# Kernel tuning notes

Hardware: AMD Instinct MI355X
Metric: run time of the kernel (lower is better)

Reference implementation:

```python
import jax, jax.numpy as jnp
import numpy as np

N_NODES = 50000
N_EDGES = 400000
IN_CH = 109
OUT_CH = 32


def setup_inputs() -> dict:
    key = jax.random.key(0)
    ks = jax.random.split(key, 12)
    dims = [(IN_CH, 10 * OUT_CH), (10 * OUT_CH, 2 * OUT_CH), (2 * OUT_CH, OUT_CH), (2 * OUT_CH, OUT_CH)]
    inp = {
        'x': jax.random.normal(ks[0], (N_NODES, IN_CH), dtype=jnp.float32),
        'edge_index': jax.random.randint(ks[1], (2, N_EDGES), 0, N_NODES, dtype=jnp.int64) if jax.config.jax_enable_x64 else jax.random.randint(ks[1], (2, N_EDGES), 0, N_NODES, dtype=jnp.int32),
    }
    names = ['W1', 'b1', 'W2', 'b2', 'Wmu', 'bmu', 'Wls', 'bls']
    for i, (fi, fo) in enumerate(dims):
        scale = 1.0 / np.sqrt(fi)
        inp[names[2 * i]] = jax.random.uniform(ks[2 + 2 * i], (fi, fo), minval=-scale, maxval=scale, dtype=jnp.float32)
        inp[names[2 * i + 1]] = jnp.zeros((fo,), dtype=jnp.float32)
    return inp


def _gcn_conv(x, src, dst, norm, W, b, n):
    # PyG GCNConv: h = x @ W, then symmetric-normalized aggregation, then + b
    h = x @ W                                   # [N, F_out]
    msg = h[src] * norm[:, None]                # [E+N, F_out]
    out = jax.ops.segment_sum(msg, dst, num_segments=n)
    return out + b


def _norm_and_loops(edge_index, n):
    # add self loops, compute D^{-1/2}(A+I)D^{-1/2} edge weights
    loops = jnp.arange(n, dtype=edge_index.dtype)
    src = jnp.concatenate([edge_index[0], loops])
    dst = jnp.concatenate([edge_index[1], loops])
    deg = jax.ops.segment_sum(jnp.ones_like(src, dtype=jnp.float32), dst, num_segments=n)
    dinv = jnp.where(deg > 0, jax.lax.rsqrt(jnp.maximum(deg, 1.0)), 0.0)
    norm = dinv[src] * dinv[dst]
    return src, dst, norm


def reference(x, edge_index, W1, b1, W2, b2, Wmu, bmu, Wls, bls):
    n = x.shape[0]
    src, dst, norm = _norm_and_loops(edge_index, n)
    h = jax.nn.relu(_gcn_conv(x, src, dst, norm, W1, b1, n))
    h = jax.nn.relu(_gcn_conv(h, src, dst, norm, W2, b2, n))
    mu = _gcn_conv(h, src, dst, norm, Wmu, bmu, n)
    logstd = _gcn_conv(h, src, dst, norm, Wls, bls, n)
    return (mu, logstd)
```

## Files before the change

### kernel.cpp

```cpp
#include <hip/hip_runtime.h>

#define NN 50000
#define NE 400000

typedef __attribute__((ext_vector_type(8))) short short8v;
typedef __attribute__((ext_vector_type(4))) float f32x4;

__device__ __forceinline__ unsigned short f2bf_rtn(float x) {
    unsigned u = __float_as_uint(x);
    unsigned r = u + 0x7FFFu + ((u >> 16) & 1u);
    return (unsigned short)(r >> 16);
}
__device__ __forceinline__ float bf2f(unsigned short h) {
    return __uint_as_float(((unsigned)h) << 16);
}

__global__ void prep_kernel(const float* __restrict__ x,
                            const float* __restrict__ W1, const float* __restrict__ W2,
                            const float* __restrict__ Wmu, const float* __restrict__ Wls,
                            unsigned* __restrict__ xp, int* __restrict__ zero_base,
                            unsigned short* __restrict__ w1t_hi,
                            unsigned short* __restrict__ w2t_hi, unsigned short* __restrict__ w2t_lo,
                            unsigned short* __restrict__ wct_hi, unsigned short* __restrict__ wct_lo) {
    int b = blockIdx.x, tid = threadIdx.x;
    if (b < 12500) {
        int idx = b * 256 + tid;
        int i = idx >> 6, c2 = (idx & 63) * 2;
        long xb = (long)i * 109;
        float v0 = (c2 < 109) ? x[xb + c2] : 0.0f;
        float v1 = (c2 + 1 < 109) ? x[xb + c2 + 1] : 0.0f;
        xp[idx] = (unsigned)f2bf_rtn(v0) | ((unsigned)f2bf_rtn(v1) << 16);
    } else if (b < 12891) {
        int i = (b - 12500) * 256 + tid;
        if (i < 100096) zero_base[i] = 0;
    } else if (b < 13051) {
        int idx = (b - 12891) * 256 + tid;
        int n = idx >> 7, k = idx & 127;
        float v = (k < 109) ? W1[(long)k * 320 + n] : 0.0f;
        w1t_hi[idx] = f2bf_rtn(v);
    } else if (b < 13131) {
        int idx = (b - 13051) * 256 + tid;
        int n = idx / 320, k = idx - n * 320;
        float v = W2[(long)k * 64 + n];
        unsigned short hb = f2bf_rtn(v);
        w2t_hi[idx] = hb;
        w2t_lo[idx] = f2bf_rtn(v - bf2f(hb));
    } else {
        int idx = (b - 13131) * 256 + tid;
        int n = idx >> 6, k = idx & 63;
        float v = (n < 32) ? Wmu[k * 32 + n] : Wls[k * 32 + (n - 32)];
        unsigned short hb = f2bf_rtn(v);
        wct_hi[idx] = hb;
        wct_lo[idx] = f2bf_rtn(v - bf2f(hb));
    }
}

__global__ void hist_kernel(const int* __restrict__ dst, int* __restrict__ counts) {
    for (int e = blockIdx.x * blockDim.x + threadIdx.x; e < NE; e += gridDim.x * blockDim.x)
        atomicAdd(&counts[dst[e]], 1);
}

__global__ void dinv_scan1_kernel(const int* __restrict__ counts, float* __restrict__ dinv,
                                  int* __restrict__ rowstart, int* __restrict__ bsum) {
    __shared__ int tmp[256];
    int tid = threadIdx.x;
    int i = blockIdx.x * 256 + tid;
    int v = (i < NN) ? counts[i] : 0;
    if (i < NN) dinv[i] = rsqrtf((float)(v + 1));
    tmp[tid] = v;
    __syncthreads();
    for (int off = 1; off < 256; off <<= 1) {
        int t = 0;
        if (tid >= off) t = tmp[tid - off];
        __syncthreads();
        if (tid >= off) tmp[tid] += t;
        __syncthreads();
    }
    if (i < NN) rowstart[i] = tmp[tid] - v;
    if (tid == 255) bsum[blockIdx.x] = tmp[255];
}

__global__ void scan23_kernel(int* __restrict__ rowstart, const int* __restrict__ bsum) {
    __shared__ int red[4];
    int tid = threadIdx.x;
    int v = (tid < 196 && tid < (int)blockIdx.x) ? bsum[tid] : 0;
    for (int off = 32; off > 0; off >>= 1) v += __shfl_down(v, off, 64);
    if ((tid & 63) == 0) red[tid >> 6] = v;
    __syncthreads();
    int pref = red[0] + red[1] + red[2] + red[3];
    int i = blockIdx.x * 256 + tid;
    if (i < NN) rowstart[i] += pref;
    if (i == 0) rowstart[NN] = NE;
}

__global__ void scatter_kernel(const int* __restrict__ src, const int* __restrict__ dst,
                               const int* __restrict__ rowstart, int* __restrict__ cursor,
                               int* __restrict__ esrc) {
    for (int e = blockIdx.x * blockDim.x + threadIdx.x; e < NE; e += gridDim.x * blockDim.x) {
        int d = dst[e];
        int pos = rowstart[d] + atomicAdd(&cursor[d], 1);
        esrc[pos] = src[e];
    }
}

__global__ __launch_bounds__(256) void agg109_packed_kernel(const int* __restrict__ rowstart,
                                                            const int* __restrict__ esrc,
                                                            const float* __restrict__ dinv,
                                                            const unsigned* __restrict__ xp,
                                                            unsigned* __restrict__ xa_hi32) {
    int wave = blockIdx.x * (blockDim.x >> 6) + (threadIdx.x >> 6);
    if (wave >= NN) return;
    int lane = threadIdx.x & 63;
    float wd = dinv[wave];
    unsigned pself = xp[(long)wave * 64 + lane];
    float acc0 = __uint_as_float(pself << 16) * wd;
    float acc1 = __uint_as_float(pself & 0xFFFF0000u) * wd;
    int j0 = rowstart[wave], j1 = rowstart[wave + 1];
    int j = j0;
    for (; j + 8 <= j1; j += 8) {
        int s[8];
        float w[8];
        unsigned pp[8];
        #pragma unroll
        for (int u = 0; u < 8; ++u) s[u] = esrc[j + u];
        #pragma unroll
        for (int u = 0; u < 8; ++u) w[u] = dinv[s[u]];
        #pragma unroll
        for (int u = 0; u < 8; ++u) pp[u] = xp[(long)s[u] * 64 + lane];
        #pragma unroll
        for (int u = 0; u < 8; ++u) {
            acc0 = fmaf(__uint_as_float(pp[u] << 16), w[u], acc0);
            acc1 = fmaf(__uint_as_float(pp[u] & 0xFFFF0000u), w[u], acc1);
        }
    }
    for (; j + 4 <= j1; j += 4) {
        int s0 = esrc[j], s1 = esrc[j + 1], s2 = esrc[j + 2], s3 = esrc[j + 3];
        float w0 = dinv[s0], w1 = dinv[s1], w2 = dinv[s2], w3 = dinv[s3];
        unsigned p0 = xp[(long)s0 * 64 + lane], p1 = xp[(long)s1 * 64 + lane];
        unsigned p2 = xp[(long)s2 * 64 + lane], p3 = xp[(long)s3 * 64 + lane];
        acc0 = fmaf(__uint_as_float(p0 << 16), w0, acc0);
        acc1 = fmaf(__uint_as_float(p0 & 0xFFFF0000u), w0, acc1);
        acc0 = fmaf(__uint_as_float(p1 << 16), w1, acc0);
        acc1 = fmaf(__uint_as_float(p1 & 0xFFFF0000u), w1, acc1);
        acc0 = fmaf(__uint_as_float(p2 << 16), w2, acc0);
        acc1 = fmaf(__uint_as_float(p2 & 0xFFFF0000u), w2, acc1);
        acc0 = fmaf(__uint_as_float(p3 << 16), w3, acc0);
        acc1 = fmaf(__uint_as_float(p3 & 0xFFFF0000u), w3, acc1);
    }
    for (; j < j1; ++j) {
        int s = esrc[j];
        float w = dinv[s];
        unsigned pv = xp[(long)s * 64 + lane];
        acc0 = fmaf(__uint_as_float(pv << 16), w, acc0);
        acc1 = fmaf(__uint_as_float(pv & 0xFFFF0000u), w, acc1);
    }
    acc0 *= wd;
    acc1 *= wd;
    xa_hi32[(long)wave * 64 + lane] =
        (unsigned)f2bf_rtn(acc0) | ((unsigned)f2bf_rtn(acc1) << 16);
}

__global__ __launch_bounds__(256) void agg64_relu_bf16_kernel(const int* __restrict__ rowstart,
                                                              const int* __restrict__ esrc,
                                                              const float* __restrict__ dinv,
                                                              const unsigned short* __restrict__ g,
                                                              const float* __restrict__ b,
                                                              unsigned short* __restrict__ hhi) {
    int wave = blockIdx.x * (blockDim.x >> 6) + (threadIdx.x >> 6);
    if (wave >= NN) return;
    int lane = threadIdx.x & 63;
    long base = (long)wave * 64;
    float acc = bf2f(g[base + lane]);
    int j0 = rowstart[wave], j1 = rowstart[wave + 1];
    int j = j0;
    for (; j + 4 <= j1; j += 4) {
        int s0 = esrc[j], s1 = esrc[j + 1], s2 = esrc[j + 2], s3 = esrc[j + 3];
        float p0 = bf2f(g[(long)s0 * 64 + lane]), p1 = bf2f(g[(long)s1 * 64 + lane]);
        float p2 = bf2f(g[(long)s2 * 64 + lane]), p3 = bf2f(g[(long)s3 * 64 + lane]);
        acc += p0 + p1 + p2 + p3;
    }
    for (; j < j1; ++j) acc += bf2f(g[(long)esrc[j] * 64 + lane]);
    float v = acc * dinv[wave] + b[lane];
    v = v > 0.0f ? v : 0.0f;
    hhi[base + lane] = f2bf_rtn(v);
}

__global__ __launch_bounds__(256) void agg64b_kernel(const int* __restrict__ rowstart,
                                                     const int* __restrict__ esrc,
                                                     const float* __restrict__ dinv,
                                                     const unsigned short* __restrict__ h,
                                                     unsigned short* __restrict__ a_hi) {
    int wave = blockIdx.x * (blockDim.x >> 6) + (threadIdx.x >> 6);
    if (wave >= NN) return;
    int lane = threadIdx.x & 63;
    long base = (long)wave * 64;
    float wd = dinv[wave];
    float acc = bf2f(h[base + lane]) * wd;
    int j0 = rowstart[wave], j1 = rowstart[wave + 1];
    int j = j0;
    for (; j + 4 <= j1; j += 4) {
        int s0 = esrc[j], s1 = esrc[j + 1], s2 = esrc[j + 2], s3 = esrc[j + 3];
        float w0 = dinv[s0], w1 = dinv[s1], w2 = dinv[s2], w3 = dinv[s3];
        float p0 = bf2f(h[(long)s0 * 64 + lane]), p1 = bf2f(h[(long)s1 * 64 + lane]);
        float p2 = bf2f(h[(long)s2 * 64 + lane]), p3 = bf2f(h[(long)s3 * 64 + lane]);
        acc = fmaf(p0, w0, acc); acc = fmaf(p1, w1, acc);
        acc = fmaf(p2, w2, acc); acc = fmaf(p3, w3, acc);
    }
    for (; j < j1; ++j) {
        int s = esrc[j];
        acc = fmaf(bf2f(h[(long)s * 64 + lane]), dinv[s], acc);
    }
    a_hi[base + lane] = f2bf_rtn(acc * wd);
}

#define LDT 72

template <int MODE>
__global__ __launch_bounds__(256) void mfma_gemm_kernel(
    const unsigned short* __restrict__ Ahi,
    const unsigned short* __restrict__ Bhi, const unsigned short* __restrict__ Blo,
    const float* __restrict__ bias, const float* __restrict__ bias2,
    const float* __restrict__ dinv,
    unsigned short* __restrict__ Chi,
    float* __restrict__ Cf, int M, int N, int K, int grid_n) {
    constexpr bool BLO = (MODE != 0);
    __shared__ unsigned short As[64 * LDT];
    __shared__ unsigned short Bs[(BLO ? 2 : 1) * 64 * LDT];
    int tid = threadIdx.x;
    int wid = tid >> 6, lane = tid & 63;
    int l15 = lane & 15, l4 = lane >> 4;

    int T = gridDim.x;
    int xcd = blockIdx.x & 7, jj = blockIdx.x >> 3;
    int q = T >> 3, r = T & 7;
    int start = (xcd < r) ? xcd * (q + 1) : r * (q + 1) + (xcd - r) * q;
    int lin = start + jj;
    int bm = lin / grid_n, bn = lin - bm * grid_n;
    int bm0 = bm * 64, bn0 = bn * 64;

    f32x4 acc[4] = {};

    for (int kc = 0; kc < K; kc += 64) {
        #pragma unroll
        for (int r2 = 0; r2 < 2; ++r2) {
            int idx = tid + 256 * r2;
            int row = idx >> 3, slot = idx & 7;
            int grow = bm0 + row;
            if (grow >= M) grow = M - 1;
            long go = (long)grow * K + kc + slot * 8;
            *(uint4*)&As[row * LDT + slot * 8] = *(const uint4*)&Ahi[go];
            long gob = (long)(bn0 + row) * K + kc + slot * 8;
            *(uint4*)&Bs[row * LDT + slot * 8] = *(const uint4*)&Bhi[gob];
            if (BLO) *(uint4*)&Bs[64 * LDT + row * LDT + slot * 8] = *(const uint4*)&Blo[gob];
        }
        __syncthreads();
        #pragma unroll
        for (int ks = 0; ks < 2; ++ks) {
            int koff = ks * 32 + l4 * 8;
            int ra = (wid * 16 + l15) * LDT + koff;
            short8v ah = *(const short8v*)&As[ra];
            #pragma unroll
            for (int n = 0; n < 4; ++n) {
                int rb = (n * 16 + l15) * LDT + koff;
                short8v bh = *(const short8v*)&Bs[rb];
                acc[n] = __builtin_amdgcn_mfma_f32_16x16x32_bf16(ah, bh, acc[n], 0, 0, 0);
                if (BLO) {
                    short8v bl = *(const short8v*)&Bs[64 * LDT + rb];
                    acc[n] = __builtin_amdgcn_mfma_f32_16x16x32_bf16(ah, bl, acc[n], 0, 0, 0);
                }
            }
        }
        __syncthreads();
    }
    int rbase = bm0 + wid * 16 + l4 * 4;
    #pragma unroll
    for (int q2 = 0; q2 < 4; ++q2) {
        int grow = rbase + q2;
        if (grow >= M) continue;
        float rs = (MODE == 1) ? dinv[grow] : 0.0f;
        #pragma unroll
        for (int n = 0; n < 4; ++n) {
            int gcol = bn0 + n * 16 + l15;
            float v = acc[n][q2];
            if (MODE == 0) {
                v += bias[gcol];
                v = v > 0.0f ? v : 0.0f;
                Chi[(long)grow * N + gcol] = f2bf_rtn(v);
            } else if (MODE == 1) {
                Chi[(long)grow * N + gcol] = f2bf_rtn(v * rs);
            } else {
                if (gcol < 32)
                    Cf[(long)grow * 32 + gcol] = v + bias[gcol];
                else
                    Cf[(long)NN * 32 + (long)grow * 32 + (gcol - 32)] = v + bias2[gcol - 32];
            }
        }
    }
}

extern "C" void kernel_launch(void* const* d_in, const int* in_sizes, int n_in,
                              void* d_out, int out_size, void* d_ws, size_t ws_size,
                              hipStream_t stream) {
    const float* x   = (const float*)d_in[0];
    const int*   ei  = (const int*)d_in[1];
    const int*   src = ei;
    const int*   dst = ei + NE;
    const float* W1  = (const float*)d_in[2];
    const float* b1  = (const float*)d_in[3];
    const float* W2  = (const float*)d_in[4];
    const float* b2  = (const float*)d_in[5];
    const float* Wmu = (const float*)d_in[6];
    const float* bmu = (const float*)d_in[7];
    const float* Wls = (const float*)d_in[8];
    const float* bls = (const float*)d_in[9];
    float* out = (float*)d_out;

    char* p = (char*)d_ws;
    float* dinv   = (float*)p; p += 50048 * 4;
    int* counts   = (int*)p;   p += 50048 * 4;
    int* cursor   = (int*)p;   p += 50048 * 4;
    int* rowstart = (int*)p;   p += 50056 * 4;
    int* bsum     = (int*)p;   p += 256 * 4;
    int* esrc     = (int*)p;   p += 400000 * 4;
    unsigned* xp          = (unsigned*)p;       p += 50000L * 64 * 4;
    unsigned short* xa_hi = (unsigned short*)p; p += 50000L * 128 * 2;
    unsigned short* a2_hi = (unsigned short*)p; p += 50000L * 64 * 2;
    unsigned short* g2b   = (unsigned short*)p; p += 50000L * 64 * 2;
    unsigned short* h1_hi = (unsigned short*)p; p += 50000L * 320 * 2;
    unsigned short* w1t_hi = (unsigned short*)p; p += 320 * 128 * 2;
    unsigned short* w2t_hi = (unsigned short*)p; p += 64 * 320 * 2;
    unsigned short* w2t_lo = (unsigned short*)p; p += 64 * 320 * 2;
    unsigned short* wct_hi = (unsigned short*)p; p += 64 * 64 * 2;
    unsigned short* wct_lo = (unsigned short*)p; p += 64 * 64 * 2;
    unsigned short* h2_hi = xa_hi;

    const int TB = 256;
    const int NB_NODES = (NN + TB - 1) / TB;
    const int NB_AGG = (NN * 64 + TB - 1) / TB;

    prep_kernel<<<13147, TB, 0, stream>>>(x, W1, W2, Wmu, Wls, xp, counts,
                                          w1t_hi, w2t_hi, w2t_lo, wct_hi, wct_lo);
    hist_kernel<<<1024, TB, 0, stream>>>(dst, counts);
    dinv_scan1_kernel<<<NB_NODES, TB, 0, stream>>>(counts, dinv, rowstart, bsum);
    scan23_kernel<<<NB_NODES, TB, 0, stream>>>(rowstart, bsum);
    scatter_kernel<<<1024, TB, 0, stream>>>(src, dst, rowstart, cursor, esrc);

    agg109_packed_kernel<<<NB_AGG, TB, 0, stream>>>(rowstart, esrc, dinv, xp,
                                                    (unsigned*)xa_hi);
    mfma_gemm_kernel<0><<<782 * 5, 256, 0, stream>>>(xa_hi, w1t_hi, nullptr, b1,
                                                     nullptr, nullptr, h1_hi, nullptr,
                                                     NN, 320, 128, 5);

    mfma_gemm_kernel<1><<<782, 256, 0, stream>>>(h1_hi, w2t_hi, w2t_lo, nullptr,
                                                 nullptr, dinv, g2b, nullptr,
                                                 NN, 64, 320, 1);
    agg64_relu_bf16_kernel<<<NB_AGG, TB, 0, stream>>>(rowstart, esrc, dinv, g2b, b2, h2_hi);

    agg64b_kernel<<<NB_AGG, TB, 0, stream>>>(rowstart, esrc, dinv, h2_hi, a2_hi);
    mfma_gemm_kernel<3><<<782, 256, 0, stream>>>(a2_hi, wct_hi, wct_lo, bmu,
                                                 bls, nullptr, nullptr, out,
                                                 NN, 64, 64, 1);
}
```

Before: 177.9 us.

## Drop bf16 lo-split weights in GEMMs and unroll aggregation loops by eight

Removes the hi/lo bf16 split of the W2 and fused mu/logstd weights, so those GEMMs run one MFMA per fragment instead of two and load half the B data into shared memory. Separately, the two 64-wide aggregation kernels get an 8-way unrolled gather loop to keep more independent loads in flight. The precision drop adds rounding error to the weights, which could loosen accuracy against the fp32 reference.

```diff
diff --git a/kernel.cpp b/kernel.cpp
--- a/kernel.cpp
+++ b/kernel.cpp
@@ -20,8 +20,8 @@
                             const float* __restrict__ Wmu, const float* __restrict__ Wls,
                             unsigned* __restrict__ xp, int* __restrict__ zero_base,
                             unsigned short* __restrict__ w1t_hi,
-                            unsigned short* __restrict__ w2t_hi, unsigned short* __restrict__ w2t_lo,
-                            unsigned short* __restrict__ wct_hi, unsigned short* __restrict__ wct_lo) {
+                            unsigned short* __restrict__ w2t_hi,
+                            unsigned short* __restrict__ wct_hi) {
     int b = blockIdx.x, tid = threadIdx.x;
     if (b < 12500) {
         int idx = b * 256 + tid;
@@ -41,17 +41,12 @@
     } else if (b < 13131) {
         int idx = (b - 13051) * 256 + tid;
         int n = idx / 320, k = idx - n * 320;
-        float v = W2[(long)k * 64 + n];
-        unsigned short hb = f2bf_rtn(v);
-        w2t_hi[idx] = hb;
-        w2t_lo[idx] = f2bf_rtn(v - bf2f(hb));
+        w2t_hi[idx] = f2bf_rtn(W2[(long)k * 64 + n]);
     } else {
         int idx = (b - 13131) * 256 + tid;
         int n = idx >> 6, k = idx & 63;
         float v = (n < 32) ? Wmu[k * 32 + n] : Wls[k * 32 + (n - 32)];
-        unsigned short hb = f2bf_rtn(v);
-        wct_hi[idx] = hb;
-        wct_lo[idx] = f2bf_rtn(v - bf2f(hb));
+        wct_hi[idx] = f2bf_rtn(v);
     }
 }
 
@@ -173,6 +168,16 @@
     float acc = bf2f(g[base + lane]);
     int j0 = rowstart[wave], j1 = rowstart[wave + 1];
     int j = j0;
+    for (; j + 8 <= j1; j += 8) {
+        int s[8];
+        float pp[8];
+        #pragma unroll
+        for (int u = 0; u < 8; ++u) s[u] = esrc[j + u];
+        #pragma unroll
+        for (int u = 0; u < 8; ++u) pp[u] = bf2f(g[(long)s[u] * 64 + lane]);
+        #pragma unroll
+        for (int u = 0; u < 8; ++u) acc += pp[u];
+    }
     for (; j + 4 <= j1; j += 4) {
         int s0 = esrc[j], s1 = esrc[j + 1], s2 = esrc[j + 2], s3 = esrc[j + 3];
         float p0 = bf2f(g[(long)s0 * 64 + lane]), p1 = bf2f(g[(long)s1 * 64 + lane]);
@@ -198,6 +203,18 @@
     float acc = bf2f(h[base + lane]) * wd;
     int j0 = rowstart[wave], j1 = rowstart[wave + 1];
     int j = j0;
+    for (; j + 8 <= j1; j += 8) {
+        int s[8];
+        float w[8], pp[8];
+        #pragma unroll
+        for (int u = 0; u < 8; ++u) s[u] = esrc[j + u];
+        #pragma unroll
+        for (int u = 0; u < 8; ++u) w[u] = dinv[s[u]];
+        #pragma unroll
+        for (int u = 0; u < 8; ++u) pp[u] = bf2f(h[(long)s[u] * 64 + lane]);
+        #pragma unroll
+        for (int u = 0; u < 8; ++u) acc = fmaf(pp[u], w[u], acc);
+    }
     for (; j + 4 <= j1; j += 4) {
         int s0 = esrc[j], s1 = esrc[j + 1], s2 = esrc[j + 2], s3 = esrc[j + 3];
         float w0 = dinv[s0], w1 = dinv[s1], w2 = dinv[s2], w3 = dinv[s3];
@@ -218,14 +235,13 @@
 template <int MODE>
 __global__ __launch_bounds__(256) void mfma_gemm_kernel(
     const unsigned short* __restrict__ Ahi,
-    const unsigned short* __restrict__ Bhi, const unsigned short* __restrict__ Blo,
+    const unsigned short* __restrict__ Bhi,
     const float* __restrict__ bias, const float* __restrict__ bias2,
     const float* __restrict__ dinv,
     unsigned short* __restrict__ Chi,
     float* __restrict__ Cf, int M, int N, int K, int grid_n) {
-    constexpr bool BLO = (MODE != 0);
     __shared__ unsigned short As[64 * LDT];
-    __shared__ unsigned short Bs[(BLO ? 2 : 1) * 64 * LDT];
+    __shared__ unsigned short Bs[64 * LDT];
     int tid = threadIdx.x;
     int wid = tid >> 6, lane = tid & 63;
     int l15 = lane & 15, l4 = lane >> 4;
@@ -251,7 +267,6 @@
             *(uint4*)&As[row * LDT + slot * 8] = *(const uint4*)&Ahi[go];
             long gob = (long)(bn0 + row) * K + kc + slot * 8;
             *(uint4*)&Bs[row * LDT + slot * 8] = *(const uint4*)&Bhi[gob];
-            if (BLO) *(uint4*)&Bs[64 * LDT + row * LDT + slot * 8] = *(const uint4*)&Blo[gob];
         }
         __syncthreads();
         #pragma unroll
@@ -264,10 +279,6 @@
                 int rb = (n * 16 + l15) * LDT + koff;
                 short8v bh = *(const short8v*)&Bs[rb];
                 acc[n] = __builtin_amdgcn_mfma_f32_16x16x32_bf16(ah, bh, acc[n], 0, 0, 0);
-                if (BLO) {
-                    short8v bl = *(const short8v*)&Bs[64 * LDT + rb];
-                    acc[n] = __builtin_amdgcn_mfma_f32_16x16x32_bf16(ah, bl, acc[n], 0, 0, 0);
-                }
             }
         }
         __syncthreads();
@@ -329,9 +340,7 @@
     unsigned short* h1_hi = (unsigned short*)p; p += 50000L * 320 * 2;
     unsigned short* w1t_hi = (unsigned short*)p; p += 320 * 128 * 2;
     unsigned short* w2t_hi = (unsigned short*)p; p += 64 * 320 * 2;
-    unsigned short* w2t_lo = (unsigned short*)p; p += 64 * 320 * 2;
     unsigned short* wct_hi = (unsigned short*)p; p += 64 * 64 * 2;
-    unsigned short* wct_lo = (unsigned short*)p; p += 64 * 64 * 2;
     unsigned short* h2_hi = xa_hi;
 
     const int TB = 256;
@@ -339,7 +348,7 @@
     const int NB_AGG = (NN * 64 + TB - 1) / TB;
 
     prep_kernel<<<13147, TB, 0, stream>>>(x, W1, W2, Wmu, Wls, xp, counts,
-                                          w1t_hi, w2t_hi, w2t_lo, wct_hi, wct_lo);
+                                          w1t_hi, w2t_hi, wct_hi);
     hist_kernel<<<1024, TB, 0, stream>>>(dst, counts);
     dinv_scan1_kernel<<<NB_NODES, TB, 0, stream>>>(counts, dinv, rowstart, bsum);
     scan23_kernel<<<NB_NODES, TB, 0, stream>>>(rowstart, bsum);
@@ -347,17 +356,17 @@
 
     agg109_packed_kernel<<<NB_AGG, TB, 0, stream>>>(rowstart, esrc, dinv, xp,
                                                     (unsigned*)xa_hi);
-    mfma_gemm_kernel<0><<<782 * 5, 256, 0, stream>>>(xa_hi, w1t_hi, nullptr, b1,
-                                                     nullptr, nullptr, h1_hi, nullptr,
+    mfma_gemm_kernel<0><<<782 * 5, 256, 0, stream>>>(xa_hi, w1t_hi, b1, nullptr,
+                                                     nullptr, h1_hi, nullptr,
                                                      NN, 320, 128, 5);
 
-    mfma_gemm_kernel<1><<<782, 256, 0, stream>>>(h1_hi, w2t_hi, w2t_lo, nullptr,
-                                                 nullptr, dinv, g2b, nullptr,
+    mfma_gemm_kernel<1><<<782, 256, 0, stream>>>(h1_hi, w2t_hi, nullptr, nullptr,
+                                                 dinv, g2b, nullptr,
                                                  NN, 64, 320, 1);
     agg64_relu_bf16_kernel<<<NB_AGG, TB, 0, stream>>>(rowstart, esrc, dinv, g2b, b2, h2_hi);
 
     agg64b_kernel<<<NB_AGG, TB, 0, stream>>>(rowstart, esrc, dinv, h2_hi, a2_hi);
-    mfma_gemm_kernel<3><<<782, 256, 0, stream>>>(a2_hi, wct_hi, wct_lo, bmu,
-                                                 bls, nullptr, nullptr, out,
+    mfma_gemm_kernel<3><<<782, 256, 0, stream>>>(a2_hi, wct_hi, bmu, bls,
+                                                 nullptr, nullptr, out,
                                                  NN, 64, 64, 1);
 }
```

Result: faster. 169.5 us (-4.7%).
